# Kernel tuning notes

Measured on AMD Instinct MI355X. Metric: run time of the kernel, lower is better.

Reference implementation:

```python
import jax, jax.numpy as jnp
import numpy as np
from jax import lax

B, D = 512, 256
C = 10  # hidden conv channels


def setup_inputs() -> dict:
    key = jax.random.key(0)
    ks = jax.random.split(key, 9)
    x = jax.random.normal(ks[0], (B, D, D), jnp.float32)
    w1 = jax.random.normal(ks[1], (C, 1, 1, 1), jnp.float32) * 0.1   # Conv2d(1,10,1)
    b1 = jax.random.normal(ks[2], (C,), jnp.float32) * 0.01
    w2 = jax.random.normal(ks[3], (1, C, 3, 3), jnp.float32) * 0.05  # Conv2d(10,1,3,1,1)
    b2 = jax.random.normal(ks[4], (1,), jnp.float32) * 0.01
    fc1_w = jax.random.normal(ks[5], (4, D * B), jnp.float32) * (1.0 / np.sqrt(D * B))
    fc1_b = jax.random.normal(ks[6], (4,), jnp.float32) * 0.01
    fc2_w = jax.random.normal(ks[7], (2, 4), jnp.float32) * 0.5
    fc2_b = jax.random.normal(ks[8], (2,), jnp.float32) * 0.01
    return {"x": x, "w1": w1, "b1": b1, "w2": w2, "b2": b2,
            "fc1_w": fc1_w, "fc1_b": fc1_b, "fc2_w": fc2_w, "fc2_b": fc2_b}


def reference(x, w1, b1, w2, b2, fc1_w, fc1_b, fc2_w, fc2_b):
    # edge-to-edge: E[b,i,j] = row_sum(i) + col_sum(j)
    rs = x.sum(axis=-1)          # [B, D]
    cs = x.sum(axis=-2)          # [B, D]
    e = (rs[:, :, None] + cs[:, None, :])[:, None]  # [B, 1, D, D]
    # Conv2d(1, C, 1) == per-pixel scale+bias over channels
    h = jax.nn.relu(e * w1.reshape(1, C, 1, 1) + b1.reshape(1, C, 1, 1))  # [B, C, D, D]
    # convSym: lower-triangular mask each channel
    h = h * jnp.tril(jnp.ones((D, D), jnp.float32))
    # Conv2d(C, 1, 3, stride=1, pad=1)
    y = lax.conv_general_dilated(h, w2, (1, 1), 'SAME',
                                 dimension_numbers=('NCHW', 'OIHW', 'NCHW'))
    y = jax.nn.relu(y + b2.reshape(1, 1, 1, 1))[:, 0]  # [B, D, D]
    # edge-to-vertex: v[b,i] = row_sum + col_sum
    v = y.sum(axis=-1) + y.sum(axis=-2)  # [B, D]
    flat = v.reshape(-1)                  # [B*D]
    hfc = jax.nn.relu(fc1_w @ flat + fc1_b)
    return fc2_w @ hfc + fc2_b            # [2]
```

## Files before the change

kernel.cpp:

```cpp
#include <hip/hip_runtime.h>

#define DD 256
#define BB 512

#define OFF_RS   0
#define OFF_CSP  131072
#define OFF_HFC  655360
#define OFF_PAR  655368
#define OFF_TABP 655384
#define OFF_TABO 655648

typedef float v2f __attribute__((ext_vector_type(2)));

__device__ __forceinline__ v2f mk2(float a, float b) { v2f r; r.x = a; r.y = b; return r; }

__device__ __forceinline__ v2f fma2(v2f a, v2f b, v2f c) {
#if __has_builtin(__builtin_elementwise_fma)
  return __builtin_elementwise_fma(a, b, c);
#else
  return mk2(fmaf(a.x, b.x, c.x), fmaf(a.y, b.y, c.y));
#endif
}

__device__ __forceinline__ float wave_red(float v) {
#pragma unroll
  for (int off = 32; off > 0; off >>= 1) v += __shfl_down(v, off, 64);
  return v;
}

__device__ __forceinline__ float rfl(float v) {
  return __uint_as_float(__builtin_amdgcn_readfirstlane(__float_as_uint(v)));
}

__global__ __launch_bounds__(256) void sum_kernel(const float* __restrict__ x,
                                                  const float* __restrict__ w1,
                                                  const float* __restrict__ b1,
                                                  const float* __restrict__ w2,
                                                  float* __restrict__ ws) {
  const int bq = blockIdx.x;
  const int tid = threadIdx.x;
  if (bq == 2048) {
    const int t = tid;
    float w1v[10], b1v[10], bp[10];
    int rank[10];
#pragma unroll
    for (int c = 0; c < 10; ++c) { w1v[c] = w1[c]; b1v[c] = b1[c]; bp[c] = -b1v[c] / w1v[c]; }
#pragma unroll
    for (int c = 0; c < 10; ++c) {
      int r = 0;
#pragma unroll
      for (int k = 0; k < 10; ++k)
        r += (bp[k] < bp[c] || (bp[k] == bp[c] && k < c)) ? 1 : 0;
      rank[c] = r;
    }
    float lo = bp[0], hi = bp[0];
#pragma unroll
    for (int c = 1; c < 10; ++c) { lo = fminf(lo, bp[c]); hi = fmaxf(hi, bp[c]); }
    if (t == 0) { ws[OFF_PAR] = lo; ws[OFF_PAR + 1] = hi; }
    if (t >= 16 && t < 26) ws[OFF_PAR + 2 + (t - 16)] = bp[t - 16];
    if (t < 99) {
      const int s = t / 9, tt = t % 9;
      const int dr = tt / 3, kc = tt % 3;
      float A = 0.f, Bv = 0.f;
      for (int c = 0; c < 10; ++c) {
        bool act = (w1v[c] > 0.f) ? (rank[c] < s)
                 : ((w1v[c] < 0.f) ? (rank[c] >= s) : (b1v[c] > 0.f));
        if (act) { A += w1v[c] * w2[c * 9 + tt]; Bv += b1v[c] * w2[c * 9 + tt]; }
      }
      float A0 = 0.f, B0 = 0.f;
      for (int c = 0; c < 10; ++c) {
        bool act0 = (w1v[c] < 0.f) || (w1v[c] == 0.f && b1v[c] > 0.f);
        if (act0) { A0 += w1v[c] * w2[c * 9 + tt]; B0 += b1v[c] * w2[c * 9 + tt]; }
      }
      const int base = (s * 3 + kc) * 8;
      const int posA = (dr == 2) ? 4 : dr;
      const int posB = (dr == 2) ? 5 : (2 + dr);
      ws[OFF_TABO + base + posA] = A;
      ws[OFF_TABO + base + posB] = Bv;
      ws[OFF_TABP + base + posA] = A - A0;
      ws[OFF_TABP + base + posB] = Bv - B0;
      ws[OFF_TABO + base + 6] = 0.f; ws[OFF_TABO + base + 7] = 0.f;
      ws[OFF_TABP + base + 6] = 0.f; ws[OFF_TABP + base + 7] = 0.f;
    }
    return;
  }
  const int b = bq >> 2;
  const int q = bq & 3;
  const int lane = tid & 63;
  const int wv = tid >> 6;
  __shared__ float rowp[64][65];
  __shared__ float csl[4][DD];
  __shared__ float segp[4][64];
  float4 cacc = make_float4(0.f, 0.f, 0.f, 0.f);
  const float4* px = (const float4*)(x + ((size_t)b << 16) + ((size_t)(q * 64 + wv * 16) << 8));
#pragma unroll
  for (int r = 0; r < 16; ++r) {
    float4 val = px[r * 64 + lane];
    cacc.x += val.x; cacc.y += val.y; cacc.z += val.z; cacc.w += val.w;
    rowp[wv * 16 + r][lane] = (val.x + val.y) + (val.z + val.w);
  }
  ((float4*)csl[wv])[lane] = cacc;
  __syncthreads();
  {
    const int row = tid & 63, seg = tid >> 6;
    const float* rp = rowp[row] + seg * 16;
    float s = 0.f;
#pragma unroll
    for (int k = 0; k < 16; ++k) s += rp[k];
    segp[seg][row] = s;
  }
  __syncthreads();
  if (tid < 64)
    ws[OFF_RS + b * DD + q * 64 + tid] =
        (segp[0][tid] + segp[1][tid]) + (segp[2][tid] + segp[3][tid]);
  ws[OFF_CSP + bq * DD + tid] =
      (csl[0][tid] + csl[1][tid]) + (csl[2][tid] + csl[3][tid]);
  if (bq == 0 && tid < 4) ws[OFF_HFC + tid] = 0.f;
}

__global__ __launch_bounds__(512, 6) void conv_kernel(const float* __restrict__ b2p,
                                                      const float* __restrict__ fc1w,
                                                      float* __restrict__ ws) {
  const int b = blockIdx.x >> 1;
  const int h = blockIdx.x & 1;
  const int tid = threadIdx.x;
  const int w = tid >> 6;
  const int lane = tid & 63;
  const int run = (h << 3) | w;

  int wb, r0, r1;
  switch (run) {
    case 0:  wb = 0; r0 = 0;   r1 = 43;  break;
    case 1:  wb = 0; r0 = 43;  r1 = 86;  break;
    case 2:  wb = 0; r0 = 86;  r1 = 129; break;
    case 3:  wb = 0; r0 = 129; r1 = 172; break;
    case 4:  wb = 0; r0 = 172; r1 = 214; break;
    case 5:  wb = 0; r0 = 214; r1 = 256; break;
    case 6:  wb = 1; r0 = 62;  r1 = 101; break;
    case 7:  wb = 1; r0 = 101; r1 = 140; break;
    case 8:  wb = 1; r0 = 140; r1 = 179; break;
    case 9:  wb = 1; r0 = 179; r1 = 218; break;
    case 10: wb = 1; r0 = 218; r1 = 256; break;
    case 11: wb = 2; r0 = 126; r1 = 170; break;
    case 12: wb = 2; r0 = 170; r1 = 213; break;
    case 13: wb = 2; r0 = 213; r1 = 256; break;
    case 14: wb = 3; r0 = 190; r1 = 223; break;
    default: wb = 3; r0 = 223; r1 = 256; break;
  }
  const int jmin = wb * 64;
  const int j = jmin + lane;
  const int dlim = jmin + 63;

  __shared__ __align__(16) float tabD_s[264];
  __shared__ __align__(16) float tabO_s[264];
  __shared__ float rs_s[DD];
  __shared__ float cs_s[DD];
  __shared__ __align__(16) float wkA[DD][4];
  __shared__ float segsum_s[4][4];
  __shared__ float red_s[32];

  const float* par = ws + OFF_PAR;
  const float lo_s = rfl(par[0]);
  const float hi_s = rfl(par[1]);
  float bp_r[10];
#pragma unroll
  for (int c = 0; c < 10; ++c) bp_r[c] = rfl(par[2 + c]);
  float dH[3][6];
  {
    const float* dhp = ws + OFF_TABP + 240;
#pragma unroll
    for (int kc = 0; kc < 3; ++kc)
#pragma unroll
      for (int m = 0; m < 6; ++m) dH[kc][m] = rfl(dhp[kc * 8 + m]);
  }

  if (tid < 256) {
    rs_s[tid] = ws[OFF_RS + b * DD + tid];
#pragma unroll
    for (int k = 0; k < 4; ++k) wkA[tid][k] = fc1w[k * (BB * DD) + b * DD + tid];
  } else {
    const int t = tid - 256;
    const float* csp = ws + OFF_CSP + (b * 4) * DD + t;
    cs_s[t] = (csp[0] + csp[DD]) + (csp[2 * DD] + csp[3 * DD]);
  }
  if (tid < 264) { tabD_s[tid] = ws[OFF_TABP + tid]; tabO_s[tid] = ws[OFF_TABO + tid]; }
  __syncthreads();
  if (tid < 16) {
    const int ss = tid >> 2, k = tid & 3;
    float s = 0.f;
#pragma unroll
    for (int r = 0; r < 64; ++r) s += wkA[ss * 64 + r][k];
    segsum_s[ss][k] = s;
  }
  __syncthreads();

  const float b2v = b2p[0];
  const float yb = fmaxf(b2v, 0.f);

  float csr[3], vf[3];
  csr[0] = (j >= 1) ? cs_s[j - 1] : 0.f;
  csr[1] = cs_s[j];
  csr[2] = (j < DD - 1) ? cs_s[j + 1] : 0.f;
  vf[0] = (j >= 1) ? 1.f : 0.f;
  vf[1] = 1.f;
  vf[2] = (j < DD - 1) ? 1.f : 0.f;
  v2f vf2[3];
#pragma unroll
  for (int kc = 0; kc < 3; ++kc) vf2[kc] = mk2(vf[kc], vf[kc]);

  v2f al01 = mk2(0.f, 0.f), be01 = mk2(0.f, 0.f);
  float al2 = 0.f, be2 = 0.f;
  {
    const float* lop = ws + OFF_TABO;
#pragma unroll
    for (int kc = 0; kc < 3; ++kc) {
      const float A0 = rfl(lop[kc * 8 + 0]), A1 = rfl(lop[kc * 8 + 1]);
      const float B0 = rfl(lop[kc * 8 + 2]), B1 = rfl(lop[kc * 8 + 3]);
      const float A2 = rfl(lop[kc * 8 + 4]), B2 = rfl(lop[kc * 8 + 5]);
      const v2f a = mk2(A0, A1);
      al01 = fma2(vf2[kc], a, al01);
      be01 = fma2(vf2[kc], fma2(a, mk2(csr[kc], csr[kc]), mk2(B0, B1)), be01);
      al2 = fmaf(vf[kc], A2, al2);
      be2 = fmaf(vf[kc], fmaf(A2, csr[kc], B2), be2);
    }
  }

  const int iend = (r1 == DD) ? DD - 1 : r1;
  float P = 0.f, Q = 0.f;
  float vcol = 0.f;
  v2f a01 = mk2(0.f, 0.f);
  v2f a23 = mk2(0.f, 0.f);

  auto fast_eval = [&](float rsv, v2f& R01, float& R2) {
    R01 = fma2(al01, mk2(rsv, rsv), be01);
    R2 = fmaf(al2, rsv, be2);
    int ia = 0;
#pragma unroll
    for (int kc = 0; kc < 3; ++kc) {
      const float e = rsv + csr[kc];
      const bool hib = e > hi_s;
      const v2f tv = fma2(mk2(e, e), mk2(dH[kc][0], dH[kc][1]), mk2(dH[kc][2], dH[kc][3]));
      const v2f mh2 = hib ? vf2[kc] : mk2(0.f, 0.f);
      R01 = fma2(mh2, tv, R01);
      const float t2 = fmaf(e, dH[kc][4], dH[kc][5]);
      R2 = fmaf(hib ? vf[kc] : 0.f, t2, R2);
      ia |= (!hib && (e > lo_s)) ? 1 : 0;
    }
    if (__any(ia)) {
#pragma unroll
      for (int kc = 0; kc < 3; ++kc) {
        const float e = rsv + csr[kc];
        if ((e > lo_s) && (e <= hi_s)) {
          int s = 0;
#pragma unroll
          for (int c = 0; c < 10; ++c) s += (bp_r[c] < e) ? 1 : 0;
          const char* tp = (const char*)tabD_s + s * 96 + kc * 32;
          const float4 ab = *(const float4*)tp;
          const float2 ab2 = *(const float2*)(tp + 16);
          const v2f tv = fma2(mk2(ab.x, ab.y), mk2(e, e), mk2(ab.z, ab.w));
          R01 = fma2(vf2[kc], tv, R01);
          R2 = fmaf(vf[kc], fmaf(ab2.x, e, ab2.y), R2);
        }
      }
    }
  };

  auto guard_eval = [&](float rsv, int i, v2f& R01, float& R2) {
#pragma unroll
    for (int kc = 0; kc < 3; ++kc) {
      const float e = rsv + csr[kc];
      const float m = ((j - 1 + kc) <= i) ? vf[kc] : 0.f;
      int s = 0;
#pragma unroll
      for (int c = 0; c < 10; ++c) s += (bp_r[c] < e) ? 1 : 0;
      const char* tp = (const char*)tabO_s + s * 96 + kc * 32;
      const float4 ab = *(const float4*)tp;
      const float2 ab2 = *(const float2*)(tp + 16);
      const v2f tv = fma2(mk2(ab.x, ab.y), mk2(e, e), mk2(ab.z, ab.w));
      R01 = fma2(mk2(m, m), tv, R01);
      R2 = fmaf(m, fmaf(ab2.x, e, ab2.y), R2);
    }
  };

  auto finalize = [&](int i, float R2v) {
    const float yd = fmaxf(P + R2v + b2v, 0.f) - yb;
    vcol += yd;
    const float4 wkv = *(const float4*)wkA[i - 1];
    a01 = fma2(mk2(yd, yd), mk2(wkv.x, wkv.y), a01);
    a23 = fma2(mk2(yd, yd), mk2(wkv.z, wkv.w), a23);
  };

  if (r0 >= dlim + 2) {
    for (int i = r0 - 1; i <= r0; ++i) {
      v2f R01; float R2;
      fast_eval(rs_s[i], R01, R2);
      P = Q + R01.y; Q = R01.x;
    }
    for (int i = r0 + 1; i <= iend; ++i) {
      v2f R01; float R2;
      fast_eval(rs_s[i], R01, R2);
      finalize(i, R2);
      P = Q + R01.y; Q = R01.x;
    }
  } else {
    const int ibeg = (r0 == 0) ? 0 : r0 - 1;
    const int ffrom = r0 + 1;
    const int gend = (iend < dlim) ? iend : dlim;
    for (int i = ibeg; i <= gend; ++i) {
      v2f R01 = mk2(0.f, 0.f); float R2 = 0.f;
      if (j - 1 <= i) guard_eval(rs_s[i], i, R01, R2);
      if (i >= ffrom) finalize(i, R2);
      P = Q + R01.y; Q = R01.x;
    }
    for (int i = dlim + 1; i <= iend; ++i) {
      v2f R01; float R2;
      fast_eval(rs_s[i], R01, R2);
      finalize(i, R2);
      P = Q + R01.y; Q = R01.x;
    }
  }
  if (r1 == DD) {
    const float yd = fmaxf(P + b2v, 0.f) - yb;
    vcol += yd;
    const float4 wkv = *(const float4*)wkA[DD - 1];
    a01 = fma2(mk2(yd, yd), mk2(wkv.x, wkv.y), a01);
    a23 = fma2(mk2(yd, yd), mk2(wkv.z, wkv.w), a23);
  }

  const float4 wkj = *(const float4*)wkA[j];
  a01 = fma2(mk2(vcol, vcol), mk2(wkj.x, wkj.y), a01);
  a23 = fma2(mk2(vcol, vcol), mk2(wkj.z, wkj.w), a23);

  float acc0 = wave_red(a01.x), acc1 = wave_red(a01.y);
  float acc2 = wave_red(a23.x), acc3 = wave_red(a23.y);
  if (lane == 0) {
    red_s[w * 4 + 0] = acc0; red_s[w * 4 + 1] = acc1;
    red_s[w * 4 + 2] = acc2; red_s[w * 4 + 3] = acc3;
  }
  __syncthreads();
  if (tid < 4) {
    float s = 0.f;
#pragma unroll
    for (int wv = 0; wv < 8; ++wv) s += red_s[wv * 4 + tid];
    const float wt = (segsum_s[0][tid] + segsum_s[1][tid]) +
                     (segsum_s[2][tid] + segsum_s[3][tid]);
    s = fmaf(256.f * yb, wt, s);
    atomicAdd(&ws[OFF_HFC + tid], s);
  }
}

__global__ void fc_kernel(const float* __restrict__ fc1b, const float* __restrict__ fc2w,
                          const float* __restrict__ fc2b, const float* __restrict__ ws,
                          float* __restrict__ out) {
  if (threadIdx.x == 0 && blockIdx.x == 0) {
    float o0 = fc2b[0], o1 = fc2b[1];
#pragma unroll
    for (int k = 0; k < 4; ++k) {
      float h = fmaxf(ws[OFF_HFC + k] + fc1b[k], 0.f);
      o0 += fc2w[k] * h;
      o1 += fc2w[4 + k] * h;
    }
    out[0] = o0; out[1] = o1;
  }
}

extern "C" void kernel_launch(void* const* d_in, const int* in_sizes, int n_in,
                              void* d_out, int out_size, void* d_ws, size_t ws_size,
                              hipStream_t stream) {
  const float* x    = (const float*)d_in[0];
  const float* w1   = (const float*)d_in[1];
  const float* b1   = (const float*)d_in[2];
  const float* w2   = (const float*)d_in[3];
  const float* b2   = (const float*)d_in[4];
  const float* fc1w = (const float*)d_in[5];
  const float* fc1b = (const float*)d_in[6];
  const float* fc2w = (const float*)d_in[7];
  const float* fc2b = (const float*)d_in[8];
  float* out = (float*)d_out;
  float* ws  = (float*)d_ws;

  hipLaunchKernelGGL(sum_kernel,  dim3(2049), dim3(256), 0, stream, x, w1, b1, w2, ws);
  hipLaunchKernelGGL(conv_kernel, dim3(1024), dim3(512), 0, stream, b2, fc1w, ws);
  hipLaunchKernelGGL(fc_kernel,   dim3(1), dim3(64), 0, stream, fc1b, fc2w, fc2b, ws, out);
}
```

Measured before the change: 263.6 us.

## Replace piecewise-linear table lookup with branchless ReLU-basis sum and split conv blocks

The conv stage drops the per-segment lookup tables, the breakpoint rank search and the divergent in-range path. Instead it writes the ReLU-composed 3x3 response as a linear term plus a sum of ten hinge functions max(e - bp_c, 0) weighted by |w1|*w2, evaluated branchlessly with packed FMAs and coefficients held in registers. Conv blocks shrink from 512 to 256 threads with twice as many blocks, so the yb correction constant is halved per block. This removes LDS table loads and wave-level branching but adds about ten hinge evaluations per tap per row and raises register pressure from the coefficient arrays.

```diff
diff --git a/kernel.cpp b/kernel.cpp
--- a/kernel.cpp
+++ b/kernel.cpp
@@ -7,8 +7,8 @@
 #define OFF_CSP  131072
 #define OFF_HFC  655360
 #define OFF_PAR  655368
-#define OFF_TABP 655384
-#define OFF_TABO 655648
+#define OFF_DE   655384
+#define OFF_G    655408
 
 typedef float v2f __attribute__((ext_vector_type(2)));
 
@@ -22,14 +22,18 @@
 #endif
 }
 
+__device__ __forceinline__ v2f max2z(v2f a) {
+#if __has_builtin(__builtin_elementwise_max)
+  return __builtin_elementwise_max(a, mk2(0.f, 0.f));
+#else
+  return mk2(fmaxf(a.x, 0.f), fmaxf(a.y, 0.f));
+#endif
+}
+
 __device__ __forceinline__ float wave_red(float v) {
 #pragma unroll
   for (int off = 32; off > 0; off >>= 1) v += __shfl_down(v, off, 64);
   return v;
-}
-
-__device__ __forceinline__ float rfl(float v) {
-  return __uint_as_float(__builtin_amdgcn_readfirstlane(__float_as_uint(v)));
 }
 
 __global__ __launch_bounds__(256) void sum_kernel(const float* __restrict__ x,
@@ -41,46 +45,23 @@
   const int tid = threadIdx.x;
   if (bq == 2048) {
     const int t = tid;
-    float w1v[10], b1v[10], bp[10];
-    int rank[10];
-#pragma unroll
-    for (int c = 0; c < 10; ++c) { w1v[c] = w1[c]; b1v[c] = b1[c]; bp[c] = -b1v[c] / w1v[c]; }
-#pragma unroll
-    for (int c = 0; c < 10; ++c) {
-      int r = 0;
-#pragma unroll
-      for (int k = 0; k < 10; ++k)
-        r += (bp[k] < bp[c] || (bp[k] == bp[c] && k < c)) ? 1 : 0;
-      rank[c] = r;
-    }
-    float lo = bp[0], hi = bp[0];
-#pragma unroll
-    for (int c = 1; c < 10; ++c) { lo = fminf(lo, bp[c]); hi = fmaxf(hi, bp[c]); }
-    if (t == 0) { ws[OFF_PAR] = lo; ws[OFF_PAR + 1] = hi; }
-    if (t >= 16 && t < 26) ws[OFF_PAR + 2 + (t - 16)] = bp[t - 16];
-    if (t < 99) {
-      const int s = t / 9, tt = t % 9;
+    float w1v[10], b1v[10];
+#pragma unroll
+    for (int c = 0; c < 10; ++c) { w1v[c] = w1[c]; b1v[c] = b1[c]; }
+    if (t < 10) ws[OFF_PAR + t] = (w1v[t] != 0.f) ? (-b1v[t] / w1v[t]) : 0.f;
+    if (t < 9) {
+      float D = 0.f, E = 0.f;
+      for (int c = 0; c < 10; ++c) {
+        if (w1v[c] < 0.f) { D += w1v[c] * w2[c * 9 + t]; E += b1v[c] * w2[c * 9 + t]; }
+        else if (w1v[c] == 0.f && b1v[c] > 0.f) { E += b1v[c] * w2[c * 9 + t]; }
+      }
+      ws[OFF_DE + t * 2] = D;
+      ws[OFF_DE + t * 2 + 1] = E;
+    }
+    if (t < 90) {
+      const int c = t / 9, tt = t % 9;
       const int dr = tt / 3, kc = tt % 3;
-      float A = 0.f, Bv = 0.f;
-      for (int c = 0; c < 10; ++c) {
-        bool act = (w1v[c] > 0.f) ? (rank[c] < s)
-                 : ((w1v[c] < 0.f) ? (rank[c] >= s) : (b1v[c] > 0.f));
-        if (act) { A += w1v[c] * w2[c * 9 + tt]; Bv += b1v[c] * w2[c * 9 + tt]; }
-      }
-      float A0 = 0.f, B0 = 0.f;
-      for (int c = 0; c < 10; ++c) {
-        bool act0 = (w1v[c] < 0.f) || (w1v[c] == 0.f && b1v[c] > 0.f);
-        if (act0) { A0 += w1v[c] * w2[c * 9 + tt]; B0 += b1v[c] * w2[c * 9 + tt]; }
-      }
-      const int base = (s * 3 + kc) * 8;
-      const int posA = (dr == 2) ? 4 : dr;
-      const int posB = (dr == 2) ? 5 : (2 + dr);
-      ws[OFF_TABO + base + posA] = A;
-      ws[OFF_TABO + base + posB] = Bv;
-      ws[OFF_TABP + base + posA] = A - A0;
-      ws[OFF_TABP + base + posB] = Bv - B0;
-      ws[OFF_TABO + base + 6] = 0.f; ws[OFF_TABO + base + 7] = 0.f;
-      ws[OFF_TABP + base + 6] = 0.f; ws[OFF_TABP + base + 7] = 0.f;
+      ws[OFF_G + (kc * 10 + c) * 4 + dr] = fabsf(w1v[c]) * w2[c * 9 + tt];
     }
     return;
   }
@@ -118,15 +99,15 @@
   if (bq == 0 && tid < 4) ws[OFF_HFC + tid] = 0.f;
 }
 
-__global__ __launch_bounds__(512, 6) void conv_kernel(const float* __restrict__ b2p,
+__global__ __launch_bounds__(256, 2) void conv_kernel(const float* __restrict__ b2p,
                                                       const float* __restrict__ fc1w,
                                                       float* __restrict__ ws) {
-  const int b = blockIdx.x >> 1;
-  const int h = blockIdx.x & 1;
+  const int b = blockIdx.x >> 2;
+  const int h = blockIdx.x & 3;
   const int tid = threadIdx.x;
   const int w = tid >> 6;
   const int lane = tid & 63;
-  const int run = (h << 3) | w;
+  const int run = (h << 2) | w;
 
   int wb, r0, r1;
   switch (run) {
@@ -151,39 +132,40 @@
   const int j = jmin + lane;
   const int dlim = jmin + 63;
 
-  __shared__ __align__(16) float tabD_s[264];
-  __shared__ __align__(16) float tabO_s[264];
   __shared__ float rs_s[DD];
   __shared__ float cs_s[DD];
   __shared__ __align__(16) float wkA[DD][4];
   __shared__ float segsum_s[4][4];
-  __shared__ float red_s[32];
-
-  const float* par = ws + OFF_PAR;
-  const float lo_s = rfl(par[0]);
-  const float hi_s = rfl(par[1]);
+  __shared__ float red_s[16];
+
   float bp_r[10];
-#pragma unroll
-  for (int c = 0; c < 10; ++c) bp_r[c] = rfl(par[2 + c]);
-  float dH[3][6];
+  v2f Gp[3][10];
+  float G2[3][10];
+  v2f Dp[3], Ep[3];
+  float D2[3], E2[3];
+#pragma unroll
+  for (int c = 0; c < 10; ++c) bp_r[c] = ws[OFF_PAR + c];
+#pragma unroll
+  for (int kc = 0; kc < 3; ++kc) {
+#pragma unroll
+    for (int c = 0; c < 10; ++c) {
+      const float* gp = ws + OFF_G + (kc * 10 + c) * 4;
+      Gp[kc][c] = mk2(gp[0], gp[1]);
+      G2[kc][c] = gp[2];
+    }
+    Dp[kc] = mk2(ws[OFF_DE + kc * 2], ws[OFF_DE + (3 + kc) * 2]);
+    Ep[kc] = mk2(ws[OFF_DE + kc * 2 + 1], ws[OFF_DE + (3 + kc) * 2 + 1]);
+    D2[kc] = ws[OFF_DE + (6 + kc) * 2];
+    E2[kc] = ws[OFF_DE + (6 + kc) * 2 + 1];
+  }
+
   {
-    const float* dhp = ws + OFF_TABP + 240;
-#pragma unroll
-    for (int kc = 0; kc < 3; ++kc)
-#pragma unroll
-      for (int m = 0; m < 6; ++m) dH[kc][m] = rfl(dhp[kc * 8 + m]);
-  }
-
-  if (tid < 256) {
     rs_s[tid] = ws[OFF_RS + b * DD + tid];
+    const float* csp = ws + OFF_CSP + (b * 4) * DD + tid;
+    cs_s[tid] = (csp[0] + csp[DD]) + (csp[2 * DD] + csp[3 * DD]);
 #pragma unroll
     for (int k = 0; k < 4; ++k) wkA[tid][k] = fc1w[k * (BB * DD) + b * DD + tid];
-  } else {
-    const int t = tid - 256;
-    const float* csp = ws + OFF_CSP + (b * 4) * DD + t;
-    cs_s[t] = (csp[0] + csp[DD]) + (csp[2 * DD] + csp[3 * DD]);
-  }
-  if (tid < 264) { tabD_s[tid] = ws[OFF_TABP + tid]; tabO_s[tid] = ws[OFF_TABO + tid]; }
+  }
   __syncthreads();
   if (tid < 16) {
     const int ss = tid >> 2, k = tid & 3;
@@ -208,21 +190,23 @@
 #pragma unroll
   for (int kc = 0; kc < 3; ++kc) vf2[kc] = mk2(vf[kc], vf[kc]);
 
+  const float csrF0 = (j >= 1) ? csr[0] : -1e30f;
+  const float csrF2 = (j < DD - 1) ? csr[2] : -1e30f;
+  v2f cm02[10]; float cm1[10];
+#pragma unroll
+  for (int c = 0; c < 10; ++c) {
+    cm02[c] = mk2(csrF0 - bp_r[c], csrF2 - bp_r[c]);
+    cm1[c] = csr[1] - bp_r[c];
+  }
+
   v2f al01 = mk2(0.f, 0.f), be01 = mk2(0.f, 0.f);
   float al2 = 0.f, be2 = 0.f;
-  {
-    const float* lop = ws + OFF_TABO;
-#pragma unroll
-    for (int kc = 0; kc < 3; ++kc) {
-      const float A0 = rfl(lop[kc * 8 + 0]), A1 = rfl(lop[kc * 8 + 1]);
-      const float B0 = rfl(lop[kc * 8 + 2]), B1 = rfl(lop[kc * 8 + 3]);
-      const float A2 = rfl(lop[kc * 8 + 4]), B2 = rfl(lop[kc * 8 + 5]);
-      const v2f a = mk2(A0, A1);
-      al01 = fma2(vf2[kc], a, al01);
-      be01 = fma2(vf2[kc], fma2(a, mk2(csr[kc], csr[kc]), mk2(B0, B1)), be01);
-      al2 = fmaf(vf[kc], A2, al2);
-      be2 = fmaf(vf[kc], fmaf(A2, csr[kc], B2), be2);
-    }
+#pragma unroll
+  for (int kc = 0; kc < 3; ++kc) {
+    al01 = fma2(vf2[kc], Dp[kc], al01);
+    be01 = fma2(vf2[kc], fma2(Dp[kc], mk2(csr[kc], csr[kc]), Ep[kc]), be01);
+    al2 = fmaf(vf[kc], D2[kc], al2);
+    be2 = fmaf(vf[kc], fmaf(D2[kc], csr[kc], E2[kc]), be2);
   }
 
   const int iend = (r1 == DD) ? DD - 1 : r1;
@@ -232,37 +216,22 @@
   v2f a23 = mk2(0.f, 0.f);
 
   auto fast_eval = [&](float rsv, v2f& R01, float& R2) {
-    R01 = fma2(al01, mk2(rsv, rsv), be01);
-    R2 = fmaf(al2, rsv, be2);
-    int ia = 0;
-#pragma unroll
-    for (int kc = 0; kc < 3; ++kc) {
-      const float e = rsv + csr[kc];
-      const bool hib = e > hi_s;
-      const v2f tv = fma2(mk2(e, e), mk2(dH[kc][0], dH[kc][1]), mk2(dH[kc][2], dH[kc][3]));
-      const v2f mh2 = hib ? vf2[kc] : mk2(0.f, 0.f);
-      R01 = fma2(mh2, tv, R01);
-      const float t2 = fmaf(e, dH[kc][4], dH[kc][5]);
-      R2 = fmaf(hib ? vf[kc] : 0.f, t2, R2);
-      ia |= (!hib && (e > lo_s)) ? 1 : 0;
-    }
-    if (__any(ia)) {
-#pragma unroll
-      for (int kc = 0; kc < 3; ++kc) {
-        const float e = rsv + csr[kc];
-        if ((e > lo_s) && (e <= hi_s)) {
-          int s = 0;
-#pragma unroll
-          for (int c = 0; c < 10; ++c) s += (bp_r[c] < e) ? 1 : 0;
-          const char* tp = (const char*)tabD_s + s * 96 + kc * 32;
-          const float4 ab = *(const float4*)tp;
-          const float2 ab2 = *(const float2*)(tp + 16);
-          const v2f tv = fma2(mk2(ab.x, ab.y), mk2(e, e), mk2(ab.z, ab.w));
-          R01 = fma2(vf2[kc], tv, R01);
-          R2 = fmaf(vf[kc], fmaf(ab2.x, e, ab2.y), R2);
-        }
-      }
-    }
+    const v2f rv2 = mk2(rsv, rsv);
+    v2f S0 = mk2(0.f, 0.f), S1 = mk2(0.f, 0.f), S2 = mk2(0.f, 0.f);
+    float T0 = 0.f, T1 = 0.f, T2 = 0.f;
+#pragma unroll
+    for (int c = 0; c < 10; ++c) {
+      const v2f u02 = max2z(rv2 + cm02[c]);
+      const float u1 = fmaxf(rsv + cm1[c], 0.f);
+      S0 = fma2(mk2(u02.x, u02.x), Gp[0][c], S0);
+      S1 = fma2(mk2(u1, u1),       Gp[1][c], S1);
+      S2 = fma2(mk2(u02.y, u02.y), Gp[2][c], S2);
+      T0 = fmaf(u02.x, G2[0][c], T0);
+      T1 = fmaf(u1,    G2[1][c], T1);
+      T2 = fmaf(u02.y, G2[2][c], T2);
+    }
+    R01 = fma2(al01, rv2, be01) + ((S0 + S1) + S2);
+    R2  = fmaf(al2, rsv, be2) + ((T0 + T1) + T2);
   };
 
   auto guard_eval = [&](float rsv, int i, v2f& R01, float& R2) {
@@ -270,15 +239,16 @@
     for (int kc = 0; kc < 3; ++kc) {
       const float e = rsv + csr[kc];
       const float m = ((j - 1 + kc) <= i) ? vf[kc] : 0.f;
-      int s = 0;
-#pragma unroll
-      for (int c = 0; c < 10; ++c) s += (bp_r[c] < e) ? 1 : 0;
-      const char* tp = (const char*)tabO_s + s * 96 + kc * 32;
-      const float4 ab = *(const float4*)tp;
-      const float2 ab2 = *(const float2*)(tp + 16);
-      const v2f tv = fma2(mk2(ab.x, ab.y), mk2(e, e), mk2(ab.z, ab.w));
-      R01 = fma2(mk2(m, m), tv, R01);
-      R2 = fmaf(m, fmaf(ab2.x, e, ab2.y), R2);
+      v2f t01 = fma2(Dp[kc], mk2(e, e), Ep[kc]);
+      float t2 = fmaf(D2[kc], e, E2[kc]);
+#pragma unroll
+      for (int c = 0; c < 10; ++c) {
+        const float u = fmaxf(e - bp_r[c], 0.f);
+        t01 = fma2(mk2(u, u), Gp[kc][c], t01);
+        t2 = fmaf(u, G2[kc][c], t2);
+      }
+      R01 = fma2(mk2(m, m), t01, R01);
+      R2 = fmaf(m, t2, R2);
     }
   };
 
@@ -339,12 +309,11 @@
   }
   __syncthreads();
   if (tid < 4) {
-    float s = 0.f;
-#pragma unroll
-    for (int wv = 0; wv < 8; ++wv) s += red_s[wv * 4 + tid];
+    float s = (red_s[0 * 4 + tid] + red_s[1 * 4 + tid]) +
+              (red_s[2 * 4 + tid] + red_s[3 * 4 + tid]);
     const float wt = (segsum_s[0][tid] + segsum_s[1][tid]) +
                      (segsum_s[2][tid] + segsum_s[3][tid]);
-    s = fmaf(256.f * yb, wt, s);
+    s = fmaf(128.f * yb, wt, s);
     atomicAdd(&ws[OFF_HFC + tid], s);
   }
 }
@@ -380,6 +349,6 @@
   float* ws  = (float*)d_ws;
 
   hipLaunchKernelGGL(sum_kernel,  dim3(2049), dim3(256), 0, stream, x, w1, b1, w2, ws);
-  hipLaunchKernelGGL(conv_kernel, dim3(1024), dim3(512), 0, stream, b2, fc1w, ws);
+  hipLaunchKernelGGL(conv_kernel, dim3(2048), dim3(256), 0, stream, b2, fc1w, ws);
   hipLaunchKernelGGL(fc_kernel,   dim3(1), dim3(64), 0, stream, fc1b, fc2w, fc2b, ws, out);
 }
```

Measured after the change: 324.2 us. 1.23x slower.
